# Kernel tuning notes

Measured on AMD Instinct MI355X. Metric: run time of the kernel, lower is better.

## Reference

```python
import jax, jax.numpy as jnp
import numpy as np

NUM_HEADS = 8

def setup_inputs() -> dict:
    key = jax.random.key(0)
    ks = jax.random.split(key, 10)
    B, S, D = 4, 2048, 512
    scale = 1.0 / np.sqrt(D)
    return {
        "x": jax.random.normal(ks[0], (B, S, D), dtype=jnp.float32),
        "q": jax.random.normal(ks[1], (B, S, D), dtype=jnp.float32),
        "Wq": jax.random.normal(ks[2], (D, D), dtype=jnp.float32) * scale,
        "bq": jax.random.normal(ks[3], (D,), dtype=jnp.float32) * 0.01,
        "Wk": jax.random.normal(ks[4], (D, D), dtype=jnp.float32) * scale,
        "bk": jax.random.normal(ks[5], (D,), dtype=jnp.float32) * 0.01,
        "Wv": jax.random.normal(ks[6], (D, D), dtype=jnp.float32) * scale,
        "bv": jax.random.normal(ks[7], (D,), dtype=jnp.float32) * 0.01,
        "Wo": jax.random.normal(ks[8], (D, D), dtype=jnp.float32) * scale,
        "bo": jax.random.normal(ks[9], (D,), dtype=jnp.float32) * 0.01,
    }

def reference(x, q, Wq, bq, Wk, bk, Wv, bv, Wo, bo):
    B, S, D = x.shape
    H = NUM_HEADS
    Dh = D // H
    # Linear layers: y = x @ W.T + b (torch nn.Linear convention)
    def split_heads(t):  # [B,S,D] -> [B,H,S,Dh]
        return t.reshape(B, -1, H, Dh).transpose(0, 2, 1, 3)
    Q = split_heads(q @ Wq.T + bq)
    K = split_heads(x @ Wk.T + bk)
    V = split_heads(x @ Wv.T + bv)
    logits = jnp.einsum('bhqd,bhkd->bhqk', Q, K) / jnp.sqrt(jnp.asarray(Dh, Q.dtype))
    attn = jax.nn.softmax(logits, axis=-1)
    out = jnp.einsum('bhqk,bhkd->bhqd', attn, V)  # [B,H,S,Dh]
    concat = out.transpose(0, 2, 1, 3).reshape(B, -1, D)
    return concat @ Wo.T + bo
```

## Files before the change

kernel.cpp:

```cpp
#include <hip/hip_runtime.h>
#include <stdint.h>

typedef __bf16 bf16_t;
typedef bf16_t bf16x8 __attribute__((ext_vector_type(8)));
typedef bf16_t bf16x4 __attribute__((ext_vector_type(4)));
typedef float f32x4 __attribute__((ext_vector_type(4)));

#define DEV __device__ __forceinline__

DEV void gload_lds16(const void* g, void* l) {
  __builtin_amdgcn_global_load_lds(
      (__attribute__((address_space(1))) void*)(g),
      (__attribute__((address_space(3))) void*)(l), 16, 0, 0);
}

__global__ __launch_bounds__(256) void cvt2_kernel(
    const float* __restrict__ x, const float* __restrict__ q,
    bf16_t* __restrict__ xb, bf16_t* __restrict__ qb) {
  const float* s = blockIdx.y ? q : x;
  bf16_t* d = blockIdx.y ? qb : xb;
  int i = blockIdx.x * 256 + threadIdx.x;
  if (i < 524288) {
    const float4* sp = (const float4*)s + (size_t)i * 2;
    float4 a = sp[0], b = sp[1];
    bf16x8 o;
    o[0] = (bf16_t)a.x; o[1] = (bf16_t)a.y; o[2] = (bf16_t)a.z; o[3] = (bf16_t)a.w;
    o[4] = (bf16_t)b.x; o[5] = (bf16_t)b.y; o[6] = (bf16_t)b.z; o[7] = (bf16_t)b.w;
    *(bf16x8*)(d + (size_t)i * 8) = o;
  }
}

__global__ __launch_bounds__(256) void cvtw_kernel(
    const float* __restrict__ Wq, const float* __restrict__ Wk,
    const float* __restrict__ Wv, const float* __restrict__ Wo,
    bf16_t* __restrict__ dst) {
  int y = blockIdx.y;
  const float* s = (y == 0) ? Wq : (y == 1) ? Wk : (y == 2) ? Wv : Wo;
  bf16_t* d = dst + (size_t)y * 262144;
  int i = blockIdx.x * 256 + threadIdx.x;
  if (i < 32768) {
    const float4* sp = (const float4*)s + (size_t)i * 2;
    float4 a = sp[0], b = sp[1];
    bf16x8 o;
    o[0] = (bf16_t)a.x; o[1] = (bf16_t)a.y; o[2] = (bf16_t)a.z; o[3] = (bf16_t)a.w;
    o[4] = (bf16_t)b.x; o[5] = (bf16_t)b.y; o[6] = (bf16_t)b.z; o[7] = (bf16_t)b.w;
    *(bf16x8*)(d + (size_t)i * 8) = o;
  }
}

DEV void gemm_core(const bf16_t* __restrict__ A, const bf16_t* __restrict__ W,
                   char* smem, f32x4 (&acc)[4][4]) {
  const int tid = threadIdx.x;
  const int lane = tid & 63;
  const int wid = tid >> 6;
  const int wr = wid >> 1, wc = wid & 1;
  const int bx = blockIdx.x, by = blockIdx.y;

  uint32_t goffA[4], goffB[4], ldsoff[4];
#pragma unroll
  for (int c = 0; c < 4; ++c) {
    uint32_t o = (uint32_t)wid * 4096u + (uint32_t)c * 1024u + (uint32_t)lane * 16u;
    uint32_t row = o >> 7;
    uint32_t inner = (o & 127u) ^ ((row & 7u) << 4);
    goffA[c] = ((uint32_t)by * 128u + row) * 1024u + inner;
    goffB[c] = ((uint32_t)bx * 128u + row) * 1024u + inner;
    ldsoff[c] = o - (uint32_t)lane * 16u;
  }
  uint32_t offA[4][2], offB[4][2];
#pragma unroll
  for (int i = 0; i < 4; ++i)
#pragma unroll
    for (int kk = 0; kk < 2; ++kk) {
      uint32_t ra = (uint32_t)(wr * 64 + i * 16 + (lane & 15));
      offA[i][kk] = ra * 128u + (((uint32_t)kk * 64u + ((lane >> 4) * 16u)) ^ ((ra & 7u) << 4));
      uint32_t rb = (uint32_t)(wc * 64 + i * 16 + (lane & 15));
      offB[i][kk] = rb * 128u + (((uint32_t)kk * 64u + ((lane >> 4) * 16u)) ^ ((rb & 7u) << 4));
    }

  const char* Ab = (const char*)A;
  const char* Wb = (const char*)W;

#pragma unroll
  for (int c = 0; c < 4; ++c) {
    gload_lds16(Ab + goffA[c], smem + ldsoff[c]);
    gload_lds16(Wb + goffB[c], smem + 16384 + ldsoff[c]);
  }
  asm volatile("s_waitcnt vmcnt(0)" ::: "memory");
  __syncthreads();

#pragma unroll 1
  for (int kt = 0; kt < 8; ++kt) {
    const int buf = kt & 1;
    char* cur = smem + buf * 32768;
    if (kt < 7) {
      char* nxt = smem + (buf ^ 1) * 32768;
      uint32_t gk = (uint32_t)(kt + 1) * 128u;
#pragma unroll
      for (int c = 0; c < 4; ++c) {
        gload_lds16(Ab + goffA[c] + gk, nxt + ldsoff[c]);
        gload_lds16(Wb + goffB[c] + gk, nxt + 16384 + ldsoff[c]);
      }
    }
    bf16x8 af[4][2], bfr[4][2];
#pragma unroll
    for (int kk = 0; kk < 2; ++kk)
#pragma unroll
      for (int i = 0; i < 4; ++i) {
        af[i][kk] = *(const bf16x8*)(cur + offA[i][kk]);
        bfr[i][kk] = *(const bf16x8*)(cur + 16384 + offB[i][kk]);
      }
    __builtin_amdgcn_s_setprio(1);
#pragma unroll
    for (int kk = 0; kk < 2; ++kk)
#pragma unroll
      for (int mi = 0; mi < 4; ++mi)
#pragma unroll
        for (int nj = 0; nj < 4; ++nj)
          acc[mi][nj] = __builtin_amdgcn_mfma_f32_16x16x32_bf16(
              af[mi][kk], bfr[nj][kk], acc[mi][nj], 0, 0, 0);
    __builtin_amdgcn_s_setprio(0);
    asm volatile("s_waitcnt vmcnt(0)" ::: "memory");
    __syncthreads();
  }
}

__global__ __launch_bounds__(256) void gemm_qkv_kernel(
    const bf16_t* __restrict__ xb, const bf16_t* __restrict__ qb,
    const bf16_t* __restrict__ Wb, const float* __restrict__ bq,
    const float* __restrict__ bk, const float* __restrict__ bv,
    bf16_t* __restrict__ Qh, bf16_t* __restrict__ Kh, bf16_t* __restrict__ VT) {
  __shared__ char smem[65536];
  const int z = blockIdx.z;
  const bf16_t* A = (z == 0) ? qb : xb;
  const bf16_t* W = Wb + (size_t)z * 262144;
  const float* bias = (z == 0) ? bq : (z == 1) ? bk : bv;

  f32x4 acc[4][4] = {};
  gemm_core(A, W, smem, acc);

  const int lane = threadIdx.x & 63, wid = threadIdx.x >> 6;
  const int wr = wid >> 1, wc = wid & 1;
  const int colbase = blockIdx.x * 128 + wc * 64 + (lane & 15);
  const int rowbase = blockIdx.y * 128 + wr * 64 + ((lane >> 4) << 2);

  if (z == 2) {
#pragma unroll
    for (int nj = 0; nj < 4; ++nj) {
      int c = colbase + nj * 16;
      float bb = bias[c];
      int h = c >> 6, d = c & 63;
#pragma unroll
      for (int mi = 0; mi < 4; ++mi) {
        int r0 = rowbase + mi * 16;
        int b = r0 >> 11, s0 = r0 & 2047;
        bf16x4 v;
#pragma unroll
        for (int rr = 0; rr < 4; ++rr) v[rr] = (bf16_t)(acc[mi][nj][rr] + bb);
        *(bf16x4*)(VT + ((size_t)((b << 3) | h) * 64 + d) * 2048 + s0) = v;
      }
    }
  } else {
    bf16_t* O = (z == 0) ? Qh : Kh;
    const float scl = (z == 0) ? 0.18033688f : 1.0f;
#pragma unroll
    for (int nj = 0; nj < 4; ++nj) {
      int c = colbase + nj * 16;
      float bb = bias[c];
      int h = c >> 6, d = c & 63;
#pragma unroll
      for (int mi = 0; mi < 4; ++mi)
#pragma unroll
        for (int rr = 0; rr < 4; ++rr) {
          int r = rowbase + mi * 16 + rr;
          int b = r >> 11, s = r & 2047;
          O[((size_t)((b << 3) | h) * 2048 + s) * 64 + d] = (bf16_t)((acc[mi][nj][rr] + bb) * scl);
        }
    }
  }
}

__global__ __launch_bounds__(256) void gemm_out_kernel(
    const bf16_t* __restrict__ ctx, const bf16_t* __restrict__ Wo,
    const float* __restrict__ bo, float* __restrict__ out) {
  __shared__ char smem[65536];
  f32x4 acc[4][4] = {};
  gemm_core(ctx, Wo, smem, acc);

  const int lane = threadIdx.x & 63, wid = threadIdx.x >> 6;
  const int wr = wid >> 1, wc = wid & 1;
  const int colbase = blockIdx.x * 128 + wc * 64 + (lane & 15);
  const int rowbase = blockIdx.y * 128 + wr * 64 + ((lane >> 4) << 2);
#pragma unroll
  for (int nj = 0; nj < 4; ++nj) {
    int c = colbase + nj * 16;
    float bb = bo[c];
#pragma unroll
    for (int mi = 0; mi < 4; ++mi)
#pragma unroll
      for (int rr = 0; rr < 4; ++rr) {
        int r = rowbase + mi * 16 + rr;
        out[(size_t)r * 512 + c] = acc[mi][nj][rr] + bb;
      }
  }
}

__global__ __launch_bounds__(256, 4) void attn_kernel(
    const bf16_t* __restrict__ Qh, const bf16_t* __restrict__ Kh,
    const bf16_t* __restrict__ VT, bf16_t* __restrict__ ctx) {
  __shared__ char smem[40960];
  char* Kb = smem;
  char* Vb = smem + 16384;
  const int tid = threadIdx.x, lane = tid & 63, wid = tid >> 6;
  char* Pw = smem + 32768 + wid * 2048;
  const int qt = blockIdx.x, bh = blockIdx.y;

  const char* Kbase = (const char*)Kh + (size_t)bh * 262144;
  const char* Vbase = (const char*)VT + (size_t)bh * 262144;
  const char* Qbase = (const char*)Qh + (size_t)bh * 262144;

  bf16x8 qf[2];
  {
    int qrow = qt * 64 + wid * 16 + (lane & 15);
    qf[0] = *(const bf16x8*)(Qbase + (size_t)qrow * 128 + ((lane >> 4) * 16));
    qf[1] = *(const bf16x8*)(Qbase + (size_t)qrow * 128 + 64 + ((lane >> 4) * 16));
  }

  uint32_t kgo[2], vgo[2], lo[2];
#pragma unroll
  for (int c = 0; c < 2; ++c) {
    uint32_t o = (uint32_t)c * 4096u + (uint32_t)wid * 1024u + (uint32_t)lane * 16u;
    uint32_t row = o >> 7;
    uint32_t inner = (o & 127u) ^ ((row & 7u) << 4);
    kgo[c] = row * 128u + inner;
    vgo[c] = row * 4096u + inner;
    lo[c] = o - (uint32_t)lane * 16u;
  }

  uint32_t fro[4][2];
#pragma unroll
  for (int nj = 0; nj < 4; ++nj)
#pragma unroll
    for (int kk = 0; kk < 2; ++kk) {
      uint32_t row = (uint32_t)(nj * 16 + (lane & 15));
      fro[nj][kk] = row * 128u + (((uint32_t)kk * 64u + ((lane >> 4) * 16u)) ^ ((row & 7u) << 4));
    }

  uint32_t pwr[4], psw[4];
#pragma unroll
  for (int rr = 0; rr < 4; ++rr) {
    uint32_t prow = (uint32_t)(((lane >> 4) << 2) + rr);
    pwr[rr] = prow * 128u;
    psw[rr] = (prow & 7u) << 4;
  }
  uint32_t prd[2];
#pragma unroll
  for (int kk = 0; kk < 2; ++kk) {
    uint32_t prow = (uint32_t)(lane & 15);
    prd[kk] = prow * 128u + (((uint32_t)kk * 64u + ((lane >> 4) * 16u)) ^ ((prow & 7u) << 4));
  }

  f32x4 o_acc[4] = {};
  float m_run[4], l_part[4];
#pragma unroll
  for (int rr = 0; rr < 4; ++rr) { m_run[rr] = -1.0e30f; l_part[rr] = 0.f; }

#pragma unroll
  for (int c = 0; c < 2; ++c) {
    gload_lds16(Kbase + kgo[c], Kb + lo[c]);
    gload_lds16(Vbase + vgo[c], Vb + lo[c]);
  }
  asm volatile("s_waitcnt vmcnt(0)" ::: "memory");
  __syncthreads();

#pragma unroll 1
  for (int t = 0; t < 32; ++t) {
    const uint32_t cur = ((uint32_t)t & 1u) << 13;
    if (t < 31) {
      const uint32_t nxt = cur ^ 8192u;
      const char* Kn = Kbase + (size_t)(t + 1) * 8192;
      const char* Vn = Vbase + (size_t)(t + 1) * 128;
#pragma unroll
      for (int c = 0; c < 2; ++c) {
        gload_lds16(Kn + kgo[c], Kb + nxt + lo[c]);
        gload_lds16(Vn + vgo[c], Vb + nxt + lo[c]);
      }
    }

    f32x4 sA[4] = {};
#pragma unroll
    for (int kk = 0; kk < 2; ++kk) {
      bf16x8 kf[4];
#pragma unroll
      for (int nj = 0; nj < 4; ++nj)
        kf[nj] = *(const bf16x8*)(Kb + cur + fro[nj][kk]);
      __builtin_amdgcn_s_setprio(1);
#pragma unroll
      for (int nj = 0; nj < 4; ++nj)
        sA[nj] = __builtin_amdgcn_mfma_f32_16x16x32_bf16(qf[kk], kf[nj], sA[nj], 0, 0, 0);
      __builtin_amdgcn_s_setprio(0);
    }

    float imax[4];
    bool ok = true;
#pragma unroll
    for (int rr = 0; rr < 4; ++rr) {
      float a0 = sA[0][rr], a1 = sA[1][rr], a2 = sA[2][rr], a3 = sA[3][rr];
      float im = fmaxf(fmaxf(a0, a1), fmaxf(a2, a3));
      imax[rr] = im;
      ok = ok && (im <= m_run[rr] + 8.0f);
    }
    if (!__all(ok)) {
#pragma unroll
      for (int rr = 0; rr < 4; ++rr) {
        float mx = imax[rr];
        mx = fmaxf(mx, __shfl_xor(mx, 1));
        mx = fmaxf(mx, __shfl_xor(mx, 2));
        mx = fmaxf(mx, __shfl_xor(mx, 4));
        mx = fmaxf(mx, __shfl_xor(mx, 8));
        float mnew = fmaxf(m_run[rr], mx);
        float sc = __builtin_exp2f(m_run[rr] - mnew);
        m_run[rr] = mnew;
        l_part[rr] *= sc;
#pragma unroll
        for (int dj = 0; dj < 4; ++dj) o_acc[dj][rr] *= sc;
      }
    }

#pragma unroll
    for (int rr = 0; rr < 4; ++rr) {
      float m = m_run[rr];
      float p0 = __builtin_exp2f(sA[0][rr] - m);
      float p1 = __builtin_exp2f(sA[1][rr] - m);
      float p2 = __builtin_exp2f(sA[2][rr] - m);
      float p3 = __builtin_exp2f(sA[3][rr] - m);
      l_part[rr] += (p0 + p1) + (p2 + p3);
      char* pr = Pw + pwr[rr];
      uint32_t sw = psw[rr];
      uint32_t cb = (uint32_t)(lane & 15) * 2u;
      *(bf16_t*)(pr + ((cb)       ^ sw)) = (bf16_t)p0;
      *(bf16_t*)(pr + ((cb + 32u) ^ sw)) = (bf16_t)p1;
      *(bf16_t*)(pr + ((cb + 64u) ^ sw)) = (bf16_t)p2;
      *(bf16_t*)(pr + ((cb + 96u) ^ sw)) = (bf16_t)p3;
    }
    asm volatile("s_waitcnt lgkmcnt(0)" ::: "memory");
    __builtin_amdgcn_sched_barrier(0);

#pragma unroll
    for (int kk = 0; kk < 2; ++kk) {
      bf16x8 pf = *(const bf16x8*)(Pw + prd[kk]);
      bf16x8 vf[4];
#pragma unroll
      for (int dj = 0; dj < 4; ++dj)
        vf[dj] = *(const bf16x8*)(Vb + cur + fro[dj][kk]);
      __builtin_amdgcn_s_setprio(1);
#pragma unroll
      for (int dj = 0; dj < 4; ++dj)
        o_acc[dj] = __builtin_amdgcn_mfma_f32_16x16x32_bf16(pf, vf[dj], o_acc[dj], 0, 0, 0);
      __builtin_amdgcn_s_setprio(0);
    }

    asm volatile("s_waitcnt vmcnt(0)" ::: "memory");
    __syncthreads();
  }

  const int b = bh >> 3, h = bh & 7;
#pragma unroll
  for (int rr = 0; rr < 4; ++rr) {
    float l = l_part[rr];
    l += __shfl_xor(l, 1);
    l += __shfl_xor(l, 2);
    l += __shfl_xor(l, 4);
    l += __shfl_xor(l, 8);
    float inv = 1.0f / l;
    int qrow = qt * 64 + wid * 16 + ((lane >> 4) << 2) + rr;
    size_t base = ((size_t)(b * 2048 + qrow)) * 512 + h * 64 + (lane & 15);
#pragma unroll
    for (int dj = 0; dj < 4; ++dj)
      ctx[base + dj * 16] = (bf16_t)(o_acc[dj][rr] * inv);
  }
}

extern "C" void kernel_launch(void* const* d_in, const int* in_sizes, int n_in,
                              void* d_out, int out_size, void* d_ws, size_t ws_size,
                              hipStream_t stream) {
  const float* x  = (const float*)d_in[0];
  const float* q  = (const float*)d_in[1];
  const float* Wq = (const float*)d_in[2];
  const float* bq = (const float*)d_in[3];
  const float* Wk = (const float*)d_in[4];
  const float* bk = (const float*)d_in[5];
  const float* Wv = (const float*)d_in[6];
  const float* bv = (const float*)d_in[7];
  const float* Wo = (const float*)d_in[8];
  const float* bo = (const float*)d_in[9];

  char* ws = (char*)d_ws;
  bf16_t* xb  = (bf16_t*)(ws + 0);
  bf16_t* qb  = (bf16_t*)(ws + 8388608);
  bf16_t* Wb  = (bf16_t*)(ws + 16777216);
  bf16_t* Qh  = (bf16_t*)(ws + 18874368);
  bf16_t* Kh  = (bf16_t*)(ws + 27262976);
  bf16_t* VT  = (bf16_t*)(ws + 35651584);
  bf16_t* ctx = (bf16_t*)(ws + 44040192);

  cvt2_kernel<<<dim3(2048, 2), 256, 0, stream>>>(x, q, xb, qb);
  cvtw_kernel<<<dim3(128, 4), 256, 0, stream>>>(Wq, Wk, Wv, Wo, Wb);
  gemm_qkv_kernel<<<dim3(4, 64, 3), 256, 0, stream>>>(xb, qb, Wb, bq, bk, bv, Qh, Kh, VT);
  attn_kernel<<<dim3(32, 32), 256, 0, stream>>>(Qh, Kh, VT, ctx);
  gemm_out_kernel<<<dim3(4, 64), 256, 0, stream>>>(ctx, Wb + 3 * 262144, bo, (float*)d_out);
}
```

Before: 129.7 us.

## Rewrite attention with transposed 32x32x16 MFMA, keeping P in registers

The attention kernel now computes S^T = K·Q^T with 32x32x16 bf16 MFMAs, so each lane owns one query row and softmax max and sum need only a single cross-half shuffle. The probability matrix is repacked into MFMA B-operand fragments with lane shuffles instead of a round trip through LDS, which removes the per-wave P buffer and its LDS wait. Each block now handles 128 queries instead of 64, halving the grid and doubling K/V reuse per tile load. In exchange, register pressure rises and launch bounds drop to 2 blocks per SM, which lowers occupancy.

```diff
diff --git a/kernel.cpp b/kernel.cpp
--- a/kernel.cpp
+++ b/kernel.cpp
@@ -4,7 +4,10 @@
 typedef __bf16 bf16_t;
 typedef bf16_t bf16x8 __attribute__((ext_vector_type(8)));
 typedef bf16_t bf16x4 __attribute__((ext_vector_type(4)));
+typedef bf16_t bf16x2 __attribute__((ext_vector_type(2)));
 typedef float f32x4 __attribute__((ext_vector_type(4)));
+typedef float f32x16 __attribute__((ext_vector_type(16)));
+typedef uint32_t u32x4 __attribute__((ext_vector_type(4)));
 
 #define DEV __device__ __forceinline__
 
@@ -204,26 +207,25 @@
   }
 }
 
-__global__ __launch_bounds__(256, 4) void attn_kernel(
+__global__ __launch_bounds__(256, 2) void attn_kernel(
     const bf16_t* __restrict__ Qh, const bf16_t* __restrict__ Kh,
     const bf16_t* __restrict__ VT, bf16_t* __restrict__ ctx) {
-  __shared__ char smem[40960];
+  __shared__ char smem[32768];
   char* Kb = smem;
   char* Vb = smem + 16384;
   const int tid = threadIdx.x, lane = tid & 63, wid = tid >> 6;
-  char* Pw = smem + 32768 + wid * 2048;
+  const int l31 = lane & 31, h = lane >> 5;
   const int qt = blockIdx.x, bh = blockIdx.y;
 
   const char* Kbase = (const char*)Kh + (size_t)bh * 262144;
   const char* Vbase = (const char*)VT + (size_t)bh * 262144;
   const char* Qbase = (const char*)Qh + (size_t)bh * 262144;
 
-  bf16x8 qf[2];
-  {
-    int qrow = qt * 64 + wid * 16 + (lane & 15);
-    qf[0] = *(const bf16x8*)(Qbase + (size_t)qrow * 128 + ((lane >> 4) * 16));
-    qf[1] = *(const bf16x8*)(Qbase + (size_t)qrow * 128 + 64 + ((lane >> 4) * 16));
-  }
+  const int qrow = qt * 128 + wid * 32 + l31;
+  bf16x8 qf[4];
+#pragma unroll
+  for (int ks = 0; ks < 4; ++ks)
+    qf[ks] = *(const bf16x8*)(Qbase + (size_t)qrow * 128 + ks * 32 + h * 16);
 
   uint32_t kgo[2], vgo[2], lo[2];
 #pragma unroll
@@ -236,33 +238,15 @@
     lo[c] = o - (uint32_t)lane * 16u;
   }
 
-  uint32_t fro[4][2];
-#pragma unroll
-  for (int nj = 0; nj < 4; ++nj)
-#pragma unroll
-    for (int kk = 0; kk < 2; ++kk) {
-      uint32_t row = (uint32_t)(nj * 16 + (lane & 15));
-      fro[nj][kk] = row * 128u + (((uint32_t)kk * 64u + ((lane >> 4) * 16u)) ^ ((row & 7u) << 4));
-    }
-
-  uint32_t pwr[4], psw[4];
-#pragma unroll
-  for (int rr = 0; rr < 4; ++rr) {
-    uint32_t prow = (uint32_t)(((lane >> 4) << 2) + rr);
-    pwr[rr] = prow * 128u;
-    psw[rr] = (prow & 7u) << 4;
-  }
-  uint32_t prd[2];
-#pragma unroll
-  for (int kk = 0; kk < 2; ++kk) {
-    uint32_t prow = (uint32_t)(lane & 15);
-    prd[kk] = prow * 128u + (((uint32_t)kk * 64u + ((lane >> 4) * 16u)) ^ ((prow & 7u) << 4));
-  }
-
-  f32x4 o_acc[4] = {};
-  float m_run[4], l_part[4];
-#pragma unroll
-  for (int rr = 0; rr < 4; ++rr) { m_run[rr] = -1.0e30f; l_part[rr] = 0.f; }
+  const uint32_t swz = (uint32_t)(l31 & 7) << 4;
+  uint32_t fbase[2], fcol[4];
+#pragma unroll
+  for (int c = 0; c < 2; ++c) fbase[c] = (uint32_t)(32 * c + l31) * 128u;
+#pragma unroll
+  for (int ks = 0; ks < 4; ++ks) fcol[ks] = ((uint32_t)(ks * 32 + h * 16)) ^ swz;
+
+  f32x16 oacc[2] = {};
+  float m_run = -1.0e30f, l_part = 0.f;
 
 #pragma unroll
   for (int c = 0; c < 2; ++c) {
@@ -286,76 +270,74 @@
       }
     }
 
-    f32x4 sA[4] = {};
-#pragma unroll
-    for (int kk = 0; kk < 2; ++kk) {
-      bf16x8 kf[4];
-#pragma unroll
-      for (int nj = 0; nj < 4; ++nj)
-        kf[nj] = *(const bf16x8*)(Kb + cur + fro[nj][kk]);
+    f32x16 sT[2] = {};
+#pragma unroll
+    for (int c = 0; c < 2; ++c) {
       __builtin_amdgcn_s_setprio(1);
 #pragma unroll
-      for (int nj = 0; nj < 4; ++nj)
-        sA[nj] = __builtin_amdgcn_mfma_f32_16x16x32_bf16(qf[kk], kf[nj], sA[nj], 0, 0, 0);
+      for (int ks = 0; ks < 4; ++ks) {
+        bf16x8 kf = *(const bf16x8*)(Kb + cur + fbase[c] + fcol[ks]);
+        sT[c] = __builtin_amdgcn_mfma_f32_32x32x16_bf16(kf, qf[ks], sT[c], 0, 0, 0);
+      }
       __builtin_amdgcn_s_setprio(0);
     }
 
-    float imax[4];
-    bool ok = true;
-#pragma unroll
-    for (int rr = 0; rr < 4; ++rr) {
-      float a0 = sA[0][rr], a1 = sA[1][rr], a2 = sA[2][rr], a3 = sA[3][rr];
-      float im = fmaxf(fmaxf(a0, a1), fmaxf(a2, a3));
-      imax[rr] = im;
-      ok = ok && (im <= m_run[rr] + 8.0f);
-    }
+    float mx = sT[0][0];
+#pragma unroll
+    for (int c = 0; c < 2; ++c)
+#pragma unroll
+      for (int r = 0; r < 16; ++r) mx = fmaxf(mx, sT[c][r]);
+    mx = fmaxf(mx, __shfl_xor(mx, 32));
+    bool ok = (mx <= m_run + 8.0f);
     if (!__all(ok)) {
-#pragma unroll
-      for (int rr = 0; rr < 4; ++rr) {
-        float mx = imax[rr];
-        mx = fmaxf(mx, __shfl_xor(mx, 1));
-        mx = fmaxf(mx, __shfl_xor(mx, 2));
-        mx = fmaxf(mx, __shfl_xor(mx, 4));
-        mx = fmaxf(mx, __shfl_xor(mx, 8));
-        float mnew = fmaxf(m_run[rr], mx);
-        float sc = __builtin_exp2f(m_run[rr] - mnew);
-        m_run[rr] = mnew;
-        l_part[rr] *= sc;
-#pragma unroll
-        for (int dj = 0; dj < 4; ++dj) o_acc[dj][rr] *= sc;
-      }
-    }
-
-#pragma unroll
-    for (int rr = 0; rr < 4; ++rr) {
-      float m = m_run[rr];
-      float p0 = __builtin_exp2f(sA[0][rr] - m);
-      float p1 = __builtin_exp2f(sA[1][rr] - m);
-      float p2 = __builtin_exp2f(sA[2][rr] - m);
-      float p3 = __builtin_exp2f(sA[3][rr] - m);
-      l_part[rr] += (p0 + p1) + (p2 + p3);
-      char* pr = Pw + pwr[rr];
-      uint32_t sw = psw[rr];
-      uint32_t cb = (uint32_t)(lane & 15) * 2u;
-      *(bf16_t*)(pr + ((cb)       ^ sw)) = (bf16_t)p0;
-      *(bf16_t*)(pr + ((cb + 32u) ^ sw)) = (bf16_t)p1;
-      *(bf16_t*)(pr + ((cb + 64u) ^ sw)) = (bf16_t)p2;
-      *(bf16_t*)(pr + ((cb + 96u) ^ sw)) = (bf16_t)p3;
-    }
-    asm volatile("s_waitcnt lgkmcnt(0)" ::: "memory");
-    __builtin_amdgcn_sched_barrier(0);
-
-#pragma unroll
-    for (int kk = 0; kk < 2; ++kk) {
-      bf16x8 pf = *(const bf16x8*)(Pw + prd[kk]);
-      bf16x8 vf[4];
-#pragma unroll
-      for (int dj = 0; dj < 4; ++dj)
-        vf[dj] = *(const bf16x8*)(Vb + cur + fro[dj][kk]);
+      float mnew = fmaxf(m_run, mx);
+      float sc = __builtin_exp2f(m_run - mnew);
+      m_run = mnew;
+      l_part *= sc;
+#pragma unroll
+      for (int r = 0; r < 16; ++r) { oacc[0][r] *= sc; oacc[1][r] *= sc; }
+    }
+
+    uint32_t cw[2][8];
+    float ladd = 0.f;
+#pragma unroll
+    for (int c = 0; c < 2; ++c)
+#pragma unroll
+      for (int w = 0; w < 8; ++w) {
+        float p0 = __builtin_exp2f(sT[c][2 * w] - m_run);
+        float p1 = __builtin_exp2f(sT[c][2 * w + 1] - m_run);
+        ladd += p0 + p1;
+        bf16x2 tp; tp[0] = (bf16_t)p0; tp[1] = (bf16_t)p1;
+        cw[c][w] = __builtin_bit_cast(uint32_t, tp);
+      }
+    l_part += ladd;
+
+    bf16x8 pa[4];
+#pragma unroll
+    for (int s = 0; s < 4; ++s) {
+      const int c = s >> 1, sp = s & 1;
+      uint32_t w0 = cw[c][4 * sp + 0], w1 = cw[c][4 * sp + 1];
+      uint32_t w2 = cw[c][4 * sp + 2], w3 = cw[c][4 * sp + 3];
+      uint32_t sx0 = (uint32_t)__shfl_xor((int)w0, 32);
+      uint32_t sx1 = (uint32_t)__shfl_xor((int)w1, 32);
+      uint32_t sx2 = (uint32_t)__shfl_xor((int)w2, 32);
+      uint32_t sx3 = (uint32_t)__shfl_xor((int)w3, 32);
+      u32x4 ta;
+      ta[0] = h ? sx2 : w0;
+      ta[1] = h ? sx3 : w1;
+      ta[2] = h ? w2 : sx0;
+      ta[3] = h ? w3 : sx1;
+      pa[s] = __builtin_bit_cast(bf16x8, ta);
+    }
+
+#pragma unroll
+    for (int dc = 0; dc < 2; ++dc) {
       __builtin_amdgcn_s_setprio(1);
 #pragma unroll
-      for (int dj = 0; dj < 4; ++dj)
-        o_acc[dj] = __builtin_amdgcn_mfma_f32_16x16x32_bf16(pf, vf[dj], o_acc[dj], 0, 0, 0);
+      for (int ks = 0; ks < 4; ++ks) {
+        bf16x8 vf = *(const bf16x8*)(Vb + cur + fbase[dc] + fcol[ks]);
+        oacc[dc] = __builtin_amdgcn_mfma_f32_32x32x16_bf16(vf, pa[ks], oacc[dc], 0, 0, 0);
+      }
       __builtin_amdgcn_s_setprio(0);
     }
 
@@ -363,21 +345,19 @@
     __syncthreads();
   }
 
-  const int b = bh >> 3, h = bh & 7;
-#pragma unroll
-  for (int rr = 0; rr < 4; ++rr) {
-    float l = l_part[rr];
-    l += __shfl_xor(l, 1);
-    l += __shfl_xor(l, 2);
-    l += __shfl_xor(l, 4);
-    l += __shfl_xor(l, 8);
-    float inv = 1.0f / l;
-    int qrow = qt * 64 + wid * 16 + ((lane >> 4) << 2) + rr;
-    size_t base = ((size_t)(b * 2048 + qrow)) * 512 + h * 64 + (lane & 15);
-#pragma unroll
-    for (int dj = 0; dj < 4; ++dj)
-      ctx[base + dj * 16] = (bf16_t)(o_acc[dj][rr] * inv);
-  }
+  float l = l_part + __shfl_xor(l_part, 32);
+  float inv = 1.0f / l;
+  const int b = bh >> 3, hh = bh & 7;
+  bf16_t* crow = ctx + ((size_t)(b * 2048 + qrow)) * 512 + hh * 64;
+#pragma unroll
+  for (int dc = 0; dc < 2; ++dc)
+#pragma unroll
+    for (int m = 0; m < 4; ++m) {
+      bf16x4 v;
+#pragma unroll
+      for (int r = 0; r < 4; ++r) v[r] = (bf16_t)(oacc[dc][4 * m + r] * inv);
+      *(bf16x4*)(crow + dc * 32 + m * 8 + h * 4) = v;
+    }
 }
 
 extern "C" void kernel_launch(void* const* d_in, const int* in_sizes, int n_in,
@@ -406,6 +386,6 @@
   cvt2_kernel<<<dim3(2048, 2), 256, 0, stream>>>(x, q, xb, qb);
   cvtw_kernel<<<dim3(128, 4), 256, 0, stream>>>(Wq, Wk, Wv, Wo, Wb);
   gemm_qkv_kernel<<<dim3(4, 64, 3), 256, 0, stream>>>(xb, qb, Wb, bq, bk, bv, Qh, Kh, VT);
-  attn_kernel<<<dim3(32, 32), 256, 0, stream>>>(Qh, Kh, VT, ctx);
+  attn_kernel<<<dim3(16, 32), 256, 0, stream>>>(Qh, Kh, VT, ctx);
   gemm_out_kernel<<<dim3(4, 64), 256, 0, stream>>>(ctx, Wb + 3 * 262144, bo, (float*)d_out);
 }
```

Measured after the change: 121.2 us. -6.5%, faster.
